# Performance work log

Measured on AMD Instinct MI355X. Metric: run time of the kernel, lower is better.

The kernel has to match this reference:

```python
import jax, jax.numpy as jnp
import numpy as np

EMBED_DIM = 512
NUM_HEADS = 8
HEAD_DIM = EMBED_DIM // NUM_HEADS


def setup_inputs() -> dict:
    key = jax.random.key(0)
    ks = jax.random.split(key, 6)
    B, S, D = 2, 4096, EMBED_DIM
    scale = 1.0 / np.sqrt(D)
    inputs = jax.random.normal(ks[0], (B, S, D), dtype=jnp.float32)
    Wq = jax.random.normal(ks[1], (D, D), dtype=jnp.float32) * scale
    Wk = jax.random.normal(ks[2], (D, D), dtype=jnp.float32) * scale
    Wv = jax.random.normal(ks[3], (D, D), dtype=jnp.float32) * scale
    Wo = jax.random.normal(ks[4], (D, D), dtype=jnp.float32) * scale
    zeros = jnp.zeros((D,), dtype=jnp.float32)
    return {"inputs": inputs, "Wq": Wq, "bq": zeros, "Wk": Wk, "bk": zeros,
            "Wv": Wv, "bv": zeros, "Wo": Wo, "bo": zeros}


def _split_heads(x, B, S):
    # [B,S,D] -> [B,H,S,hd]
    return x.reshape(B, S, NUM_HEADS, HEAD_DIM).transpose(0, 2, 1, 3)


def reference(inputs, Wq, bq, Wk, bk, Wv, bv, Wo, bo):
    B, S, D = inputs.shape
    q = _split_heads(inputs @ Wq + bq, B, S)
    k = _split_heads(inputs @ Wk + bk, B, S)
    v = _split_heads(inputs @ Wv + bv, B, S)
    scale = 1.0 / jnp.sqrt(jnp.asarray(HEAD_DIM, dtype=inputs.dtype))
    # full [B,H,S,S] score matrix, as in the original naive SDPA
    scores = jnp.einsum('bhqd,bhkd->bhqk', q, k) * scale
    weights = jax.nn.softmax(scores, axis=-1)
    attn = jnp.einsum('bhqk,bhkd->bhqd', weights, v)
    attn = attn.transpose(0, 2, 1, 3).reshape(B, S, D)
    return attn @ Wo + bo
```

## Files before the change

### kernel.cpp

```cpp
#include <hip/hip_runtime.h>
#include <hip/hip_bf16.h>
#include <stdint.h>


typedef __bf16 bf16x8 __attribute__((ext_vector_type(8)));
typedef float f32x4 __attribute__((ext_vector_type(4)));

using as1_void = __attribute__((address_space(1))) void;
using as3_void = __attribute__((address_space(3))) void;

__device__ __forceinline__ void gload16(const void* g, void* l) {
    __builtin_amdgcn_global_load_lds((const as1_void*)g, (as3_void*)l, 16, 0, 0);
}

__device__ __forceinline__ f32x4 mfma16(bf16x8 a, bf16x8 b, f32x4 c) {
    return __builtin_amdgcn_mfma_f32_16x16x32_bf16(a, b, c, 0, 0, 0);
}

__global__ void cvt_x(const float* __restrict__ in, __hip_bfloat16* __restrict__ out, int n) {
    int i = (blockIdx.x * 256 + threadIdx.x) * 4;
    if (i >= n) return;
    float4 v = *reinterpret_cast<const float4*>(in + i);
    union { __hip_bfloat16 h[4]; uint2 u; } r;
    r.h[0] = __float2bfloat16(v.x);
    r.h[1] = __float2bfloat16(v.y);
    r.h[2] = __float2bfloat16(v.z);
    r.h[3] = __float2bfloat16(v.w);
    *reinterpret_cast<uint2*>(out + i) = r.u;
}

__global__ void cvt_wt(const float* __restrict__ w0, const float* __restrict__ w1,
                       const float* __restrict__ w2, const float* __restrict__ w3,
                       __hip_bfloat16* __restrict__ o0, __hip_bfloat16* __restrict__ o1,
                       __hip_bfloat16* __restrict__ o2, __hip_bfloat16* __restrict__ o3) {
    const float* W; __hip_bfloat16* O;
    switch (blockIdx.z) {
        case 0: W = w0; O = o0; break;
        case 1: W = w1; O = o1; break;
        case 2: W = w2; O = o2; break;
        default: W = w3; O = o3; break;
    }
    __shared__ float t[32][33];
    int n0 = blockIdx.x * 32, k0 = blockIdx.y * 32;
    int tx = threadIdx.x, ty = threadIdx.y;
    for (int j = 0; j < 4; ++j)
        t[ty + 8 * j][tx] = W[(size_t)(k0 + ty + 8 * j) * 512 + n0 + tx];
    __syncthreads();
    for (int j = 0; j < 4; ++j)
        O[(size_t)(n0 + ty + 8 * j) * 512 + k0 + tx] = __float2bfloat16(t[tx][ty + 8 * j]);
}

__global__ __launch_bounds__(256, 2) void gemm_qkv(
    const __hip_bfloat16* __restrict__ A, const __hip_bfloat16* __restrict__ Bt,
    const float* __restrict__ bq, const float* __restrict__ bk, const float* __restrict__ bv,
    __hip_bfloat16* __restrict__ Qb, __hip_bfloat16* __restrict__ Kb,
    __hip_bfloat16* __restrict__ Vtb, float qs)
{
    const int K = 512;
    __shared__ __hip_bfloat16 Abuf[128 * 32];
    __shared__ __hip_bfloat16 Bbuf[128 * 32];
    const int tid = threadIdx.x, w = tid >> 6, lane = tid & 63;
    const int col = lane & 15, quad = lane >> 4;
    const int wr = w >> 1, wc = w & 1;
    const int tileN = blockIdx.x * 128, tileM = blockIdx.y * 128;

    f32x4 acc[4][4] = {};

    for (int k0 = 0; k0 < K; k0 += 32) {
        for (int i = 0; i < 2; ++i) {
            int g = w * 2 + i;
            int chunk = g * 64 + lane;
            int row = chunk >> 2, c8 = chunk & 3;
            gload16(A + (size_t)(tileM + row) * K + k0 + c8 * 8, Abuf + g * 512);
            gload16(Bt + (size_t)(tileN + row) * K + k0 + c8 * 8, Bbuf + g * 512);
        }
        __syncthreads();
        bf16x8 af[4], bfr[4];
        for (int mt = 0; mt < 4; ++mt)
            af[mt] = *reinterpret_cast<const bf16x8*>(Abuf + (wr * 64 + mt * 16 + col) * 32 + quad * 8);
        for (int nt = 0; nt < 4; ++nt)
            bfr[nt] = *reinterpret_cast<const bf16x8*>(Bbuf + (wc * 64 + nt * 16 + col) * 32 + quad * 8);
        for (int mt = 0; mt < 4; ++mt)
            for (int nt = 0; nt < 4; ++nt)
                acc[mt][nt] = mfma16(af[mt], bfr[nt], acc[mt][nt]);
        __syncthreads();
    }

    const int seg = (tileN + wc * 64) >> 9;
    const float* bias = (seg == 0) ? bq : (seg == 1) ? bk : bv;
    const float scale = (seg == 0) ? qs : 1.0f;
    __hip_bfloat16* outp = (seg == 0) ? Qb : (seg == 1) ? Kb : Vtb;

    for (int mt = 0; mt < 4; ++mt) {
        for (int nt = 0; nt < 4; ++nt) {
            int n = tileN + wc * 64 + nt * 16 + col;
            int nn = n & 511, h = nn >> 6, d = nn & 63;
            float bn = bias[nn];
            for (int r = 0; r < 4; ++r) {
                int m = tileM + wr * 64 + mt * 16 + quad * 4 + r;
                int b = m >> 12, s = m & 4095;
                float v = (acc[mt][nt][r] + bn) * scale;
                size_t off;
                if (seg < 2) off = (((size_t)(b * 8 + h) * 4096 + s) << 6) + d;
                else         off = (((size_t)(b * 8 + h) * 64 + d) << 12) + s;
                outp[off] = __float2bfloat16(v);
            }
        }
    }
}

__global__ __launch_bounds__(256, 2) void gemm_out(
    const __hip_bfloat16* __restrict__ A, const __hip_bfloat16* __restrict__ Bt,
    const float* __restrict__ bias, float* __restrict__ out)
{
    const int N = 512, K = 512;
    __shared__ __hip_bfloat16 Abuf[128 * 32];
    __shared__ __hip_bfloat16 Bbuf[128 * 32];
    const int tid = threadIdx.x, w = tid >> 6, lane = tid & 63;
    const int col = lane & 15, quad = lane >> 4;
    const int wr = w >> 1, wc = w & 1;
    const int tileN = blockIdx.x * 128, tileM = blockIdx.y * 128;

    f32x4 acc[4][4] = {};

    for (int k0 = 0; k0 < K; k0 += 32) {
        for (int i = 0; i < 2; ++i) {
            int g = w * 2 + i;
            int chunk = g * 64 + lane;
            int row = chunk >> 2, c8 = chunk & 3;
            gload16(A + (size_t)(tileM + row) * K + k0 + c8 * 8, Abuf + g * 512);
            gload16(Bt + (size_t)(tileN + row) * K + k0 + c8 * 8, Bbuf + g * 512);
        }
        __syncthreads();
        bf16x8 af[4], bfr[4];
        for (int mt = 0; mt < 4; ++mt)
            af[mt] = *reinterpret_cast<const bf16x8*>(Abuf + (wr * 64 + mt * 16 + col) * 32 + quad * 8);
        for (int nt = 0; nt < 4; ++nt)
            bfr[nt] = *reinterpret_cast<const bf16x8*>(Bbuf + (wc * 64 + nt * 16 + col) * 32 + quad * 8);
        for (int mt = 0; mt < 4; ++mt)
            for (int nt = 0; nt < 4; ++nt)
                acc[mt][nt] = mfma16(af[mt], bfr[nt], acc[mt][nt]);
        __syncthreads();
    }

    for (int mt = 0; mt < 4; ++mt) {
        for (int nt = 0; nt < 4; ++nt) {
            int n = tileN + wc * 64 + nt * 16 + col;
            float bn = bias[n];
            for (int r = 0; r < 4; ++r) {
                int m = tileM + wr * 64 + mt * 16 + quad * 4 + r;
                out[(size_t)m * N + n] = acc[mt][nt][r] + bn;
            }
        }
    }
}

__global__ __launch_bounds__(256) void flash(
    const __hip_bfloat16* __restrict__ Q,
    const __hip_bfloat16* __restrict__ Kq,
    const __hip_bfloat16* __restrict__ Vt,
    __hip_bfloat16* __restrict__ attnb)
{
    __shared__ __hip_bfloat16 KT[4096];
    __shared__ __hip_bfloat16 VB[4096];
    __shared__ __hip_bfloat16 PT[4][16 * 72];

    const int bh = blockIdx.y, b = bh >> 3, h = bh & 7;
    const int tid = threadIdx.x, w = tid >> 6, lane = tid & 63;
    const int col = lane & 15, quad = lane >> 4;
    const int q0 = blockIdx.x * 64 + w * 16;

    const __hip_bfloat16* Qh = Q + (size_t)bh * 4096 * 64;
    const __hip_bfloat16* Kh = Kq + (size_t)bh * 4096 * 64;
    const __hip_bfloat16* Vh = Vt + (size_t)bh * 64 * 4096;

    bf16x8 aq[2];
    aq[0] = *reinterpret_cast<const bf16x8*>(Qh + (size_t)(q0 + col) * 64 + quad * 8);
    aq[1] = *reinterpret_cast<const bf16x8*>(Qh + (size_t)(q0 + col) * 64 + 32 + quad * 8);

    bf16x8 ones;
    for (int j = 0; j < 8; ++j) ones[j] = (__bf16)1.0f;

    f32x4 o[4] = {};
    f32x4 acc_l = {};

    __hip_bfloat16* Pw = &PT[w][0];

    for (int kt = 0; kt < 64; ++kt) {
        for (int i = 0; i < 2; ++i) {
            int g = w * 2 + i;
            gload16(Kh + (size_t)(kt * 64 + lane) * 64 + g * 8, KT + g * 512);
            gload16(Vh + (size_t)lane * 4096 + kt * 64 + g * 8, VB + g * 512);
        }
        __syncthreads();

        f32x4 sc[4] = {};
        for (int ks = 0; ks < 2; ++ks)
            for (int nt = 0; nt < 4; ++nt) {
                bf16x8 bk = *reinterpret_cast<const bf16x8*>(KT + (ks * 4 + quad) * 512 + (nt * 16 + col) * 8);
                sc[nt] = mfma16(aq[ks], bk, sc[nt]);
            }

        for (int nt = 0; nt < 4; ++nt)
            for (int r = 0; r < 4; ++r)
                Pw[(quad * 4 + r) * 72 + nt * 16 + col] =
                    __float2bfloat16(__builtin_amdgcn_exp2f(sc[nt][r]));
        bf16x8 ap[2];
        ap[0] = *reinterpret_cast<const bf16x8*>(Pw + col * 72 + quad * 8);
        ap[1] = *reinterpret_cast<const bf16x8*>(Pw + col * 72 + 32 + quad * 8);

        for (int ks = 0; ks < 2; ++ks) {
            for (int dt = 0; dt < 4; ++dt) {
                bf16x8 bv = *reinterpret_cast<const bf16x8*>(VB + (ks * 4 + quad) * 512 + (dt * 16 + col) * 8);
                o[dt] = mfma16(ap[ks], bv, o[dt]);
            }
            acc_l = mfma16(ap[ks], ones, acc_l);
        }
        __syncthreads();
    }

    float inv[4];
    for (int r = 0; r < 4; ++r) inv[r] = 1.0f / acc_l[r];
    for (int dt = 0; dt < 4; ++dt)
        for (int r = 0; r < 4; ++r) {
            int s = q0 + quad * 4 + r;
            attnb[((size_t)b * 4096 + s) * 512 + h * 64 + dt * 16 + col] =
                __float2bfloat16(o[dt][r] * inv[r]);
        }
}

extern "C" void kernel_launch(void* const* d_in, const int* in_sizes, int n_in,
                              void* d_out, int out_size, void* d_ws, size_t ws_size,
                              hipStream_t stream) {
    const float* X  = (const float*)d_in[0];
    const float* Wq = (const float*)d_in[1];
    const float* bq = (const float*)d_in[2];
    const float* Wk = (const float*)d_in[3];
    const float* bk = (const float*)d_in[4];
    const float* Wv = (const float*)d_in[5];
    const float* bv = (const float*)d_in[6];
    const float* Wo = (const float*)d_in[7];
    const float* bo = (const float*)d_in[8];
    float* out = (float*)d_out;

    char* ws = (char*)d_ws;
    __hip_bfloat16* Xb  = (__hip_bfloat16*)(ws);
    __hip_bfloat16* Wqt = (__hip_bfloat16*)(ws + ((size_t)8 << 20));
    __hip_bfloat16* Wkt = Wqt + 512 * 512;
    __hip_bfloat16* Wvt = Wkt + 512 * 512;
    __hip_bfloat16* Wot = Wvt + 512 * 512;
    __hip_bfloat16* Qb  = (__hip_bfloat16*)(ws + ((size_t)10 << 20));
    __hip_bfloat16* Kb  = (__hip_bfloat16*)(ws + ((size_t)18 << 20));
    __hip_bfloat16* Vtb = (__hip_bfloat16*)(ws + ((size_t)26 << 20));
    __hip_bfloat16* Atb = (__hip_bfloat16*)(ws + ((size_t)34 << 20));

    const int M = 8192, K = 512;

    cvt_x<<<4096, 256, 0, stream>>>(X, Xb, M * K);
    cvt_wt<<<dim3(16, 16, 4), dim3(32, 8), 0, stream>>>(Wq, Wk, Wv, Wo, Wqt, Wkt, Wvt, Wot);

    const float qs = 0.125f * 1.4426950408889634f;
    gemm_qkv<<<dim3(12, 64), 256, 0, stream>>>(Xb, Wqt, bq, bk, bv, Qb, Kb, Vtb, qs);

    flash<<<dim3(64, 16), 256, 0, stream>>>(Qb, Kb, Vtb, Atb);

    gemm_out<<<dim3(4, 64), 256, 0, stream>>>(Atb, Wot, bo, out);
}
```

Measured before the change: 247.7 us.

## Double-buffer K/V tiles, swizzle LDS, and double queries per wave in flash kernel

The flash kernel now prefetches the next K/V tile into a second LDS buffer while computing on the current one, and drops one barrier per iteration. Each wave handles 32 queries instead of 16, so every K/V fragment read from LDS feeds twice as many MFMAs. LDS layouts use an XOR swizzle to avoid bank conflicts, and the MFMA operands are swapped so scores come out transposed with packed P writes. The output is written as vectorized stores. The cost is higher LDS and register usage and half as many blocks, which may lower occupancy.

```diff
diff --git a/kernel.cpp b/kernel.cpp
--- a/kernel.cpp
+++ b/kernel.cpp
@@ -15,6 +15,13 @@
 
 __device__ __forceinline__ f32x4 mfma16(bf16x8 a, bf16x8 b, f32x4 c) {
     return __builtin_amdgcn_mfma_f32_16x16x32_bf16(a, b, c, 0, 0, 0);
+}
+
+__device__ __forceinline__ uint32_t pkbf(float a, float b) {
+    union { __hip_bfloat16 h[2]; uint32_t u; } r;
+    r.h[0] = __float2bfloat16(a);
+    r.h[1] = __float2bfloat16(b);
+    return r.u;
 }
 
 __global__ void cvt_x(const float* __restrict__ in, __hip_bfloat16* __restrict__ out, int n) {
@@ -161,72 +168,113 @@
     const __hip_bfloat16* __restrict__ Vt,
     __hip_bfloat16* __restrict__ attnb)
 {
-    __shared__ __hip_bfloat16 KT[4096];
-    __shared__ __hip_bfloat16 VB[4096];
-    __shared__ __hip_bfloat16 PT[4][16 * 72];
+    __shared__ __hip_bfloat16 KT[2][4096];
+    __shared__ __hip_bfloat16 VB[2][4096];
+    __shared__ uint32_t TB[4][1024];
 
     const int bh = blockIdx.y, b = bh >> 3, h = bh & 7;
     const int tid = threadIdx.x, w = tid >> 6, lane = tid & 63;
     const int col = lane & 15, quad = lane >> 4;
-    const int q0 = blockIdx.x * 64 + w * 16;
+    const int q0 = blockIdx.x * 128 + w * 32;
+    const int c7 = col & 7;
 
     const __hip_bfloat16* Qh = Q + (size_t)bh * 4096 * 64;
     const __hip_bfloat16* Kh = Kq + (size_t)bh * 4096 * 64;
     const __hip_bfloat16* Vh = Vt + (size_t)bh * 64 * 4096;
 
-    bf16x8 aq[2];
-    aq[0] = *reinterpret_cast<const bf16x8*>(Qh + (size_t)(q0 + col) * 64 + quad * 8);
-    aq[1] = *reinterpret_cast<const bf16x8*>(Qh + (size_t)(q0 + col) * 64 + 32 + quad * 8);
+    bf16x8 aq[2][2];
+    for (int qh = 0; qh < 2; ++qh)
+        for (int ks = 0; ks < 2; ++ks)
+            aq[qh][ks] = *reinterpret_cast<const bf16x8*>(
+                Qh + (size_t)(q0 + qh * 16 + col) * 64 + ks * 32 + quad * 8);
+
+    const __hip_bfloat16* ksrc[2];
+    const __hip_bfloat16* vsrc[2];
+    int ldsoff[2];
+    for (int i = 0; i < 2; ++i) {
+        int c = i * 256 + tid;
+        int row = c >> 3, s8 = (c & 7) ^ (row & 7);
+        ksrc[i] = Kh + row * 64 + s8 * 8;
+        vsrc[i] = Vh + (size_t)row * 4096 + s8 * 8;
+        ldsoff[i] = (i * 256 + w * 64) * 8;
+    }
 
     bf16x8 ones;
     for (int j = 0; j < 8; ++j) ones[j] = (__bf16)1.0f;
 
-    f32x4 o[4] = {};
-    f32x4 acc_l = {};
-
-    __hip_bfloat16* Pw = &PT[w][0];
+    f32x4 o[4][2] = {};
+    f32x4 accl[2] = {};
+
+    uint32_t* TBw = &TB[w][0];
+
+    for (int i = 0; i < 2; ++i) {
+        gload16(ksrc[i], &KT[0][ldsoff[i]]);
+        gload16(vsrc[i], &VB[0][ldsoff[i]]);
+    }
+    __syncthreads();
 
     for (int kt = 0; kt < 64; ++kt) {
-        for (int i = 0; i < 2; ++i) {
-            int g = w * 2 + i;
-            gload16(Kh + (size_t)(kt * 64 + lane) * 64 + g * 8, KT + g * 512);
-            gload16(Vh + (size_t)lane * 4096 + kt * 64 + g * 8, VB + g * 512);
-        }
-        __syncthreads();
-
-        f32x4 sc[4] = {};
+        const int p = kt & 1;
+        if (kt < 63) {
+            for (int i = 0; i < 2; ++i) {
+                gload16(ksrc[i] + (size_t)(kt + 1) * 4096, &KT[1 - p][ldsoff[i]]);
+                gload16(vsrc[i] + (size_t)(kt + 1) * 64,   &VB[1 - p][ldsoff[i]]);
+            }
+        }
+
+        f32x4 sc[4][2] = {};
         for (int ks = 0; ks < 2; ++ks)
-            for (int nt = 0; nt < 4; ++nt) {
-                bf16x8 bk = *reinterpret_cast<const bf16x8*>(KT + (ks * 4 + quad) * 512 + (nt * 16 + col) * 8);
-                sc[nt] = mfma16(aq[ks], bk, sc[nt]);
-            }
-
-        for (int nt = 0; nt < 4; ++nt)
-            for (int r = 0; r < 4; ++r)
-                Pw[(quad * 4 + r) * 72 + nt * 16 + col] =
-                    __float2bfloat16(__builtin_amdgcn_exp2f(sc[nt][r]));
-        bf16x8 ap[2];
-        ap[0] = *reinterpret_cast<const bf16x8*>(Pw + col * 72 + quad * 8);
-        ap[1] = *reinterpret_cast<const bf16x8*>(Pw + col * 72 + 32 + quad * 8);
+            for (int kg = 0; kg < 4; ++kg) {
+                bf16x8 ak = *reinterpret_cast<const bf16x8*>(
+                    &KT[p][(kg * 16 + col) * 64 + (((ks * 4 + quad) ^ c7) << 3)]);
+                for (int qh = 0; qh < 2; ++qh)
+                    sc[kg][qh] = mfma16(ak, aq[qh][ks], sc[kg][qh]);
+            }
+
+        for (int kg = 0; kg < 4; ++kg)
+            for (int qh = 0; qh < 2; ++qh) {
+                f32x4 v = sc[kg][qh];
+                uint32_t u0 = pkbf(__builtin_amdgcn_exp2f(v[0]), __builtin_amdgcn_exp2f(v[1]));
+                uint32_t u1 = pkbf(__builtin_amdgcn_exp2f(v[2]), __builtin_amdgcn_exp2f(v[3]));
+                int q = qh * 16 + col;
+                int base = q * 32 + (((kg * 2 + (quad >> 1)) ^ c7) << 2) + ((quad & 1) * 2);
+                TBw[base]     = u0;
+                TBw[base + 1] = u1;
+            }
+
+        bf16x8 bp[2][2];
+        for (int qh = 0; qh < 2; ++qh)
+            for (int ks = 0; ks < 2; ++ks) {
+                int q = qh * 16 + col;
+                bp[qh][ks] = *reinterpret_cast<const bf16x8*>(
+                    &TBw[q * 32 + (((ks * 4 + quad) ^ c7) << 2)]);
+            }
 
         for (int ks = 0; ks < 2; ++ks) {
             for (int dt = 0; dt < 4; ++dt) {
-                bf16x8 bv = *reinterpret_cast<const bf16x8*>(VB + (ks * 4 + quad) * 512 + (dt * 16 + col) * 8);
-                o[dt] = mfma16(ap[ks], bv, o[dt]);
-            }
-            acc_l = mfma16(ap[ks], ones, acc_l);
-        }
-        __syncthreads();
-    }
-
-    float inv[4];
-    for (int r = 0; r < 4; ++r) inv[r] = 1.0f / acc_l[r];
-    for (int dt = 0; dt < 4; ++dt)
-        for (int r = 0; r < 4; ++r) {
-            int s = q0 + quad * 4 + r;
-            attnb[((size_t)b * 4096 + s) * 512 + h * 64 + dt * 16 + col] =
-                __float2bfloat16(o[dt][r] * inv[r]);
-        }
+                bf16x8 av = *reinterpret_cast<const bf16x8*>(
+                    &VB[p][(dt * 16 + col) * 64 + (((ks * 4 + quad) ^ c7) << 3)]);
+                for (int qh = 0; qh < 2; ++qh)
+                    o[dt][qh] = mfma16(av, bp[qh][ks], o[dt][qh]);
+            }
+            for (int qh = 0; qh < 2; ++qh)
+                accl[qh] = mfma16(ones, bp[qh][ks], accl[qh]);
+        }
+
+        __syncthreads();
+    }
+
+    for (int qh = 0; qh < 2; ++qh) {
+        float inv = 1.0f / accl[qh][0];
+        int s = q0 + qh * 16 + col;
+        __hip_bfloat16* dst = attnb + ((size_t)b * 4096 + s) * 512 + h * 64 + quad * 4;
+        for (int dt = 0; dt < 4; ++dt) {
+            union { __hip_bfloat16 hh[4]; ushort4 v4; } pk;
+            for (int r = 0; r < 4; ++r)
+                pk.hh[r] = __float2bfloat16(o[dt][qh][r] * inv);
+            *reinterpret_cast<ushort4*>(dst + dt * 16) = pk.v4;
+        }
+    }
 }
 
 extern "C" void kernel_launch(void* const* d_in, const int* in_sizes, int n_in,
@@ -262,7 +310,7 @@
     const float qs = 0.125f * 1.4426950408889634f;
     gemm_qkv<<<dim3(12, 64), 256, 0, stream>>>(Xb, Wqt, bq, bk, bv, Qb, Kb, Vtb, qs);
 
-    flash<<<dim3(64, 16), 256, 0, stream>>>(Qb, Kb, Vtb, Atb);
+    flash<<<dim3(32, 16), 256, 0, stream>>>(Qb, Kb, Vtb, Atb);
 
     gemm_out<<<dim3(4, 64), 256, 0, stream>>>(Atb, Wot, bo, out);
 }
```

New measurement: 238.3 us. -3.8%, faster.
